# Kernel tuning notes

Hardware: AMD Instinct MI355X
Metric: run time of the kernel (lower is better)

## Reference

```python
import jax, jax.numpy as jnp
import numpy as np

N = 20000      # nodes
E = 640000     # edges (before self loops)
IN = 256       # in_channels == out_channels (forced by classifier size 4*in)
H1, C1 = 8, 16   # conv1: heads=8, out=16 -> concat 128
H2, C2 = 1, 256  # conv2: heads=1, out=out_channels
B = 4096       # article pairs
NEG_SLOPE = 0.2  # PyG GATv2Conv default negative_slope


def setup_inputs() -> dict:
    key = jax.random.key(0)
    ks = jax.random.split(key, 24)
    s = 0.05
    inp = {
        "gnn_x": jax.random.normal(ks[0], (N, IN), jnp.float32),
        "vanilla_x": jax.random.normal(ks[1], (N, IN), jnp.float32),
        "edge_src": jax.random.randint(ks[2], (E,), 0, N, jnp.int32),
        "edge_dst": jax.random.randint(ks[3], (E,), 0, N, jnp.int32),
        "a1_idx": jax.random.randint(ks[4], (B,), 0, N, jnp.int64),
        "a2_idx": jax.random.randint(ks[5], (B,), 0, N, jnp.int64),
        # conv1 params (lin_l, lin_r, att, bias)
        "Wl1": jax.random.normal(ks[6], (IN, H1 * C1), jnp.float32) * s,
        "bl1": jnp.zeros((H1 * C1,), jnp.float32),
        "Wr1": jax.random.normal(ks[7], (IN, H1 * C1), jnp.float32) * s,
        "br1": jnp.zeros((H1 * C1,), jnp.float32),
        "att1": jax.random.normal(ks[8], (H1, C1), jnp.float32) * s,
        "bias1": jnp.zeros((H1 * C1,), jnp.float32),
        # conv2 params
        "Wl2": jax.random.normal(ks[9], (H1 * C1, H2 * C2), jnp.float32) * s,
        "bl2": jnp.zeros((H2 * C2,), jnp.float32),
        "Wr2": jax.random.normal(ks[10], (H1 * C1, H2 * C2), jnp.float32) * s,
        "br2": jnp.zeros((H2 * C2,), jnp.float32),
        "att2": jax.random.normal(ks[11], (H2, C2), jnp.float32) * s,
        "bias2": jnp.zeros((H2 * C2,), jnp.float32),
        # classifier
        "Wc": jax.random.normal(ks[12], (4 * IN, 1), jnp.float32) * s,
        "bc": jnp.zeros((1,), jnp.float32),
    }
    return inp


def _gatv2_layer(x, src, dst, Wl, bl, Wr, br, att, bias):
    """GATv2Conv: x_l = lin_l(x)[src], x_r = lin_r(x)[dst];
    e = att . leaky_relu(x_l + x_r); segment softmax over dst; scatter-add x_l*alpha."""
    n = x.shape[0]
    h, c = att.shape
    xl = (x @ Wl + bl).reshape(n, h, c)
    xr = (x @ Wr + br).reshape(n, h, c)
    # per-edge attention logits [E, H]
    e = jnp.einsum('ehc,hc->eh', jax.nn.leaky_relu(xl[src] + xr[dst], NEG_SLOPE), att)
    # segment softmax over destination nodes (self loops guarantee non-empty segments)
    emax = jax.ops.segment_max(e, dst, num_segments=n)
    ex = jnp.exp(e - emax[dst])
    denom = jax.ops.segment_sum(ex, dst, num_segments=n)
    alpha = ex / denom[dst]                      # [E, H]
    out = jax.ops.segment_sum(alpha[:, :, None] * xl[src], dst, num_segments=n)  # [N,H,C]
    return out.reshape(n, h * c) + bias          # concat=True (heads=1 identical)


def reference(gnn_x, vanilla_x, Wl1, bl1, Wr1, br1, att1, bias1,
              Wl2, bl2, Wr2, br2, att2, bias2, Wc, bc,
              edge_src, edge_dst, a1_idx, a2_idx):
    n = gnn_x.shape[0]
    loops = jnp.arange(n, dtype=edge_src.dtype)
    src = jnp.concatenate([edge_src, loops])     # PyG add_self_loops=True
    dst = jnp.concatenate([edge_dst, loops])
    x = _gatv2_layer(gnn_x, src, dst, Wl1, bl1, Wr1, br1, att1, bias1)
    x = jax.nn.relu(x)
    x = _gatv2_layer(x, src, dst, Wl2, bl2, Wr2, br2, att2, bias2)
    combined = jnp.concatenate(
        [vanilla_x[a1_idx], vanilla_x[a2_idx], x[a1_idx], x[a2_idx]], axis=1)  # [B, 4*IN]
    logits = combined @ Wc + bc                  # [B, 1]
    return logits
```

## Files before the change

### kernel.cpp

```cpp
#include <hip/hip_runtime.h>
#include <math.h>

#define N_NODES 20000
#define M_PAD   20032
#define E_EDGES 640000
#define ET (E_EDGES + N_NODES)
#define IN_CH 256
#define D1 128
#define D2 256
#define BPAIRS 4096
#define NEG 0.2f
#define LOG2E 1.4426950408889634f

#define ZC_BLOCKS    20
#define WT_BLOCKS    32
#define XCONV_BLOCKS (M_PAD * IN_CH / 4 / 4 / 256)
#define RANK_BLOCKS  ((ET + 255) / 256)

#define G1X (M_PAD / 64)
#define G1Y (D1 / 64)
#define G1_BLOCKS (G1X * G1Y)
#define SCAT_BLOCKS ((ET + 255) / 256)

#if __has_builtin(__builtin_amdgcn_exp2f)
#define EXP2F(x) __builtin_amdgcn_exp2f(x)
#else
#define EXP2F(x) exp2f(x)
#endif

typedef __bf16 bf16x8 __attribute__((ext_vector_type(8)));
typedef float  f32x4  __attribute__((ext_vector_type(4)));
typedef float  f32x2  __attribute__((ext_vector_type(2)));
typedef unsigned short u16x4 __attribute__((ext_vector_type(4)));

__device__ __forceinline__ unsigned short f2b(float f) {
    unsigned int u = __float_as_uint(f);
    unsigned int r = u + 0x7FFFu + ((u >> 16) & 1u);
    return (unsigned short)(r >> 16);
}
__device__ __forceinline__ unsigned char f2f8(float f) {
    return (unsigned char)(__builtin_amdgcn_cvt_pk_fp8_f32(f, f, 0, false) & 0xFF);
}
template <bool HI>
__device__ __forceinline__ f32x2 f8up2(unsigned int u) {
    return __builtin_amdgcn_cvt_pk_f32_fp8((int)u, HI);
}
__device__ __forceinline__ f32x2 up2(unsigned int u) {
    f32x2 r;
    r.x = __uint_as_float(u << 16);
    r.y = __uint_as_float(u & 0xFFFF0000u);
    return r;
}
__device__ __forceinline__ f32x2 lrelu2(f32x2 s) {
    return __builtin_elementwise_max(s, s * NEG);
}
__device__ __forceinline__ float lrelu(float s) { return fmaxf(s, NEG * s); }

__device__ __forceinline__ void unpack8(uint4 u, float* v) {
    v[0] = __uint_as_float(u.x << 16); v[1] = __uint_as_float(u.x & 0xFFFF0000u);
    v[2] = __uint_as_float(u.y << 16); v[3] = __uint_as_float(u.y & 0xFFFF0000u);
    v[4] = __uint_as_float(u.z << 16); v[5] = __uint_as_float(u.z & 0xFFFF0000u);
    v[6] = __uint_as_float(u.w << 16); v[7] = __uint_as_float(u.w & 0xFFFF0000u);
}
__device__ __forceinline__ void unpack8_f8(uint2 u, float* v) {
    f32x2 a = f8up2<false>(u.x), b = f8up2<true>(u.x);
    f32x2 c = f8up2<false>(u.y), d = f8up2<true>(u.y);
    v[0] = a.x; v[1] = a.y; v[2] = b.x; v[3] = b.y;
    v[4] = c.x; v[5] = c.y; v[6] = d.x; v[7] = d.y;
}


__global__ __launch_bounds__(256) void prep_kernel(
        const float* __restrict__ gnn_x,
        const float* __restrict__ Wl1, const float* __restrict__ Wr1,
        const float* __restrict__ Wl2, const float* __restrict__ Wr2,
        unsigned short* __restrict__ xb,
        unsigned short* __restrict__ wt1l, unsigned short* __restrict__ wt1r,
        unsigned short* __restrict__ wt2l, unsigned short* __restrict__ wt2r,
        int* __restrict__ count) {
    __shared__ unsigned short tile[64 * 65];
    int bid = blockIdx.x;
    if (bid < ZC_BLOCKS) {
        int q = bid * 256 + threadIdx.x;
        if (q * 4 < N_NODES) {
            int4 z; z.x = z.y = z.z = z.w = 0;
            ((int4*)count)[q] = z;
        }
    } else if (bid < ZC_BLOCKS + WT_BLOCKS) {
        int t = bid - ZC_BLOCKS;
        int m = t >> 3;
        int tt = t & 7;
        const float* W;
        unsigned short* Wt;
        int K, N;
        if (m == 0)      { W = Wl1; Wt = wt1l; K = IN_CH; N = D1; }
        else if (m == 1) { W = Wr1; Wt = wt1r; K = IN_CH; N = D1; }
        else if (m == 2) { W = Wl2; Wt = wt2l; K = D1; N = D2; }
        else             { W = Wr2; Wt = wt2r; K = D1; N = D2; }
        int ntn = N >> 6;
        int k0 = (tt / ntn) << 6;
        int n0 = (tt % ntn) << 6;
        int c = threadIdx.x & 63;
        int rr = threadIdx.x >> 6;
#pragma unroll
        for (int ch = 0; ch < 16; ch++) {
            int row = rr * 16 + ch;
            tile[row * 65 + c] = f2b(W[(size_t)(k0 + row) * N + n0 + c]);
        }
        __syncthreads();
#pragma unroll
        for (int ch = 0; ch < 16; ch++) {
            int n = rr * 16 + ch;
            Wt[(size_t)(n0 + n) * K + k0 + c] = tile[c * 65 + n];
        }
    } else {
        int tid = (bid - ZC_BLOCKS - WT_BLOCKS) * 256 + threadIdx.x;
        const int NQ = M_PAD * IN_CH / 4;
        int q0 = tid * 4;
#pragma unroll
        for (int j = 0; j < 4; j++) {
            int qi = q0 + j;
            if (qi >= NQ) break;
            int e0 = qi * 4;
            int row = e0 >> 8;
            u16x4 o;
            if (row < N_NODES) {
                f32x4 v = __builtin_nontemporal_load((const f32x4*)(gnn_x + e0));
                o.x = f2b(v.x); o.y = f2b(v.y); o.z = f2b(v.z); o.w = f2b(v.w);
            } else {
                o.x = o.y = o.z = o.w = 0;
            }
            *(u16x4*)(xb + e0) = o;
        }
    }
}


__global__ __launch_bounds__(256) void rank_kernel(
        const int* __restrict__ edge_dst,
        int* __restrict__ count, int* __restrict__ rank) {
    int e = blockIdx.x * 256 + threadIdx.x;
    if (e >= ET) return;
    int dst = (e < E_EDGES) ? edge_dst[e] : (e - E_EDGES);
    rank[e] = atomicAdd(&count[dst], 1);
}


__global__ __launch_bounds__(1024) void scan_kernel(const int* __restrict__ count,
                                                    int* __restrict__ offsets) {
    const int PER = 20;
    int t = threadIdx.x;
    int base = t * PER;
    int local[PER];
    int sum = 0;
#pragma unroll
    for (int i = 0; i < PER; i++) {
        int idx = base + i;
        int v = (idx < N_NODES) ? count[idx] : 0;
        local[i] = sum;
        sum += v;
    }
    int lane = t & 63, wave = t >> 6;
    int s = sum;
#pragma unroll
    for (int off = 1; off < 64; off <<= 1) {
        int x = __shfl_up(s, off);
        if (lane >= off) s += x;
    }
    __shared__ int wsum[16];
    __shared__ int wpre[16];
    if (lane == 63) wsum[wave] = s;
    __syncthreads();
    if (t == 0) {
        int acc = 0;
        for (int w = 0; w < 16; w++) { wpre[w] = acc; acc += wsum[w]; }
        offsets[N_NODES] = acc;
    }
    __syncthreads();
    int thread_excl = wpre[wave] + (s - sum);
#pragma unroll
    for (int i = 0; i < PER; i++) {
        int idx = base + i;
        if (idx < N_NODES) offsets[idx] = thread_excl + local[i];
    }
}


template <int K>
__device__ __forceinline__ void dual_gemm_tile(
        const unsigned short* __restrict__ A,
        const unsigned short* __restrict__ Wtl,
        const unsigned short* __restrict__ Wtr,
        const float* __restrict__ bl, const float* __restrict__ br,
        unsigned char* __restrict__ Yl, unsigned short* __restrict__ Yr,
        int M, int NOUT, int bx, int by) {
    const int NK = K / 32;
    int wave = threadIdx.x >> 6;
    int lane = threadIdx.x & 63;
    int row0 = bx * 64;
    int col0 = (by * 4 + wave) * 16;
    int rsub = lane & 15;
    int koff = (lane >> 4) * 8;

    const unsigned short* ap  = A   + (size_t)(row0 + rsub) * K + koff;
    const unsigned short* bpl = Wtl + (size_t)(col0 + rsub) * K + koff;
    const unsigned short* bpr = Wtr + (size_t)(col0 + rsub) * K + koff;

    bf16x8 bfl[NK], bfr[NK];
#pragma unroll
    for (int kb = 0; kb < NK; kb++) {
        bfl[kb] = *(const bf16x8*)(bpl + kb * 32);
        bfr[kb] = *(const bf16x8*)(bpr + kb * 32);
    }

    f32x4 l0 = {0.f, 0.f, 0.f, 0.f};
    f32x4 l1 = l0, l2 = l0, l3 = l0, r0 = l0, r1 = l0, r2 = l0, r3 = l0;

#pragma unroll
    for (int kb = 0; kb < NK; kb++) {
        int off = kb * 32;
        bf16x8 a0 = *(const bf16x8*)(ap + off);
        bf16x8 a1 = *(const bf16x8*)(ap + 16 * K + off);
        bf16x8 a2 = *(const bf16x8*)(ap + 32 * K + off);
        bf16x8 a3 = *(const bf16x8*)(ap + 48 * K + off);
        l0 = __builtin_amdgcn_mfma_f32_16x16x32_bf16(a0, bfl[kb], l0, 0, 0, 0);
        r0 = __builtin_amdgcn_mfma_f32_16x16x32_bf16(a0, bfr[kb], r0, 0, 0, 0);
        l1 = __builtin_amdgcn_mfma_f32_16x16x32_bf16(a1, bfl[kb], l1, 0, 0, 0);
        r1 = __builtin_amdgcn_mfma_f32_16x16x32_bf16(a1, bfr[kb], r1, 0, 0, 0);
        l2 = __builtin_amdgcn_mfma_f32_16x16x32_bf16(a2, bfl[kb], l2, 0, 0, 0);
        r2 = __builtin_amdgcn_mfma_f32_16x16x32_bf16(a2, bfr[kb], r2, 0, 0, 0);
        l3 = __builtin_amdgcn_mfma_f32_16x16x32_bf16(a3, bfl[kb], l3, 0, 0, 0);
        r3 = __builtin_amdgcn_mfma_f32_16x16x32_bf16(a3, bfr[kb], r3, 0, 0, 0);
    }

    int colg = col0 + rsub;
    float bvl = bl[colg];
    float bvr = br[colg];
    int rbase = row0 + (lane >> 4) * 4;
#pragma unroll
    for (int t = 0; t < 4; t++) {
        f32x4 al = (t == 0) ? l0 : (t == 1) ? l1 : (t == 2) ? l2 : l3;
        f32x4 ar = (t == 0) ? r0 : (t == 1) ? r1 : (t == 2) ? r2 : r3;
#pragma unroll
        for (int r = 0; r < 4; r++) {
            int row = rbase + t * 16 + r;
            if (row < M) {
                Yl[(size_t)row * NOUT + colg] = f2f8(al[r] + bvl);
                Yr[(size_t)row * NOUT + colg] = f2b(ar[r] + bvr);
            }
        }
    }
}


__global__ __launch_bounds__(256) void gemm1_scatter_kernel(
        const unsigned short* __restrict__ A,
        const unsigned short* __restrict__ Wtl,
        const unsigned short* __restrict__ Wtr,
        const float* __restrict__ bl, const float* __restrict__ br,
        unsigned char* __restrict__ Yl, unsigned short* __restrict__ Yr,
        const int* __restrict__ edge_src, const int* __restrict__ edge_dst,
        const int* __restrict__ rank, const int* __restrict__ offsets,
        int* __restrict__ sorted_src) {
    int bid = blockIdx.x;
    if (bid < G1_BLOCKS) {
        dual_gemm_tile<IN_CH>(A, Wtl, Wtr, bl, br, Yl, Yr,
                              N_NODES, D1, bid % G1X, bid / G1X);
    } else {
        int e = (bid - G1_BLOCKS) * 256 + threadIdx.x;
        if (e >= ET) return;
        int dst = (e < E_EDGES) ? edge_dst[e] : (e - E_EDGES);
        int src = (e < E_EDGES) ? edge_src[e] : (e - E_EDGES);
        sorted_src[offsets[dst] + rank[e]] = src;
    }
}


template <int K>
__global__ __launch_bounds__(256) void dual_gemm_w32_kernel(
        const unsigned short* __restrict__ A,
        const unsigned short* __restrict__ Wtl,
        const unsigned short* __restrict__ Wtr,
        const float* __restrict__ bl, const float* __restrict__ br,
        unsigned char* __restrict__ Yl, unsigned short* __restrict__ Yr,
        int M, int NOUT) {
    const int NK = K / 32;
    int wave = threadIdx.x >> 6;
    int lane = threadIdx.x & 63;
    int row0 = blockIdx.x * 64;
    int col0 = blockIdx.y * 128 + wave * 32;
    int rsub = lane & 15;
    int koff = (lane >> 4) * 8;

    const unsigned short* ap = A + (size_t)(row0 + rsub) * K + koff;

    bf16x8 bfl[2][NK], bfr[2][NK];
#pragma unroll
    for (int c = 0; c < 2; c++) {
        const unsigned short* bpl = Wtl + (size_t)(col0 + c * 16 + rsub) * K + koff;
        const unsigned short* bpr = Wtr + (size_t)(col0 + c * 16 + rsub) * K + koff;
#pragma unroll
        for (int kb = 0; kb < NK; kb++) {
            bfl[c][kb] = *(const bf16x8*)(bpl + kb * 32);
            bfr[c][kb] = *(const bf16x8*)(bpr + kb * 32);
        }
    }

    f32x4 accl[2][4], accr[2][4];
#pragma unroll
    for (int c = 0; c < 2; c++)
#pragma unroll
        for (int t = 0; t < 4; t++) {
            accl[c][t] = (f32x4){0.f, 0.f, 0.f, 0.f};
            accr[c][t] = (f32x4){0.f, 0.f, 0.f, 0.f};
        }

#pragma unroll
    for (int kb = 0; kb < NK; kb++) {
        int off = kb * 32;
        bf16x8 a[4];
        a[0] = *(const bf16x8*)(ap + off);
        a[1] = *(const bf16x8*)(ap + 16 * K + off);
        a[2] = *(const bf16x8*)(ap + 32 * K + off);
        a[3] = *(const bf16x8*)(ap + 48 * K + off);
#pragma unroll
        for (int t = 0; t < 4; t++) {
#pragma unroll
            for (int c = 0; c < 2; c++) {
                accl[c][t] = __builtin_amdgcn_mfma_f32_16x16x32_bf16(
                    a[t], bfl[c][kb], accl[c][t], 0, 0, 0);
                accr[c][t] = __builtin_amdgcn_mfma_f32_16x16x32_bf16(
                    a[t], bfr[c][kb], accr[c][t], 0, 0, 0);
            }
        }
    }

    int rbase = row0 + (lane >> 4) * 4;
#pragma unroll
    for (int c = 0; c < 2; c++) {
        int colg = col0 + c * 16 + rsub;
        float bvl = bl[colg];
        float bvr = br[colg];
#pragma unroll
        for (int t = 0; t < 4; t++) {
#pragma unroll
            for (int r = 0; r < 4; r++) {
                int row = rbase + t * 16 + r;
                if (row < M) {
                    Yl[(size_t)row * NOUT + colg] = f2f8(accl[c][t][r] + bvl);
                    Yr[(size_t)row * NOUT + colg] = f2b(accr[c][t][r] + bvr);
                }
            }
        }
    }
}


__global__ __launch_bounds__(256) void aggregate1_kernel(
        const unsigned char* __restrict__ xl1, const unsigned short* __restrict__ xr1,
        const float* __restrict__ att1, const float* __restrict__ bias1,
        const int* __restrict__ offsets, const int* __restrict__ sorted_src,
        unsigned short* __restrict__ x1) {
    int wave = threadIdx.x >> 6;
    int lane = threadIdx.x & 63;
    int q = lane >> 4;
    int ql = lane & 15;
    int dst = blockIdx.x * 4 + wave;
    if (dst >= M_PAD) return;
    int c0 = ql * 8;
    if (dst >= N_NODES) {
        if (q == 0) {
            uint4 z; z.x = z.y = z.z = z.w = 0;
            *(uint4*)(x1 + (size_t)dst * D1 + c0) = z;
        }
        return;
    }

    uint4 xu = *(const uint4*)(xr1 + (size_t)dst * D1 + c0);
    f32x2 xr[4] = {up2(xu.x), up2(xu.y), up2(xu.z), up2(xu.w)};
    float4 aa0 = *(const float4*)(att1 + c0);
    float4 aa1 = *(const float4*)(att1 + c0 + 4);
    f32x2 att[4];
    att[0].x = aa0.x * LOG2E; att[0].y = aa0.y * LOG2E;
    att[1].x = aa0.z * LOG2E; att[1].y = aa0.w * LOG2E;
    att[2].x = aa1.x * LOG2E; att[2].y = aa1.y * LOG2E;
    att[3].x = aa1.z * LOG2E; att[3].y = aa1.w * LOG2E;

    int beg = offsets[dst], end = offsets[dst + 1];
    const unsigned char* base = xl1 + c0;

    float l = 0.f;
    f32x2 acc[4] = {{0.f,0.f},{0.f,0.f},{0.f,0.f},{0.f,0.f}};

    int i = beg;
    int s0 = sorted_src[min(i + q, end - 1)];
    uint2 g0 = *(const uint2*)(base + (size_t)s0 * D1);
    bool more1 = (i + 4) < end;
    uint2 g1;
    if (more1) {
        int s1 = sorted_src[min(i + 4 + q, end - 1)];
        g1 = *(const uint2*)(base + (size_t)s1 * D1);
    }
    while (true) {
        bool more2 = (i + 8) < end;
        uint2 g2;
        if (more2) {
            int s2 = sorted_src[min(i + 8 + q, end - 1)];
            g2 = *(const uint2*)(base + (size_t)s2 * D1);
        }
        bool act = (i + q) < end;
        f32x2 v0 = f8up2<false>(g0.x), v1 = f8up2<true>(g0.x);
        f32x2 v2 = f8up2<false>(g0.y), v3 = f8up2<true>(g0.y);
        f32x2 p2 = att[0] * lrelu2(v0 + xr[0]);
        p2 += att[1] * lrelu2(v1 + xr[1]);
        p2 += att[2] * lrelu2(v2 + xr[2]);
        p2 += att[3] * lrelu2(v3 + xr[3]);
        float p = p2.x + p2.y;
        p += __shfl_xor(p, 1);
        float w = act ? EXP2F(p) : 0.f;
        l += w;
        acc[0] += w * v0; acc[1] += w * v1; acc[2] += w * v2; acc[3] += w * v3;
        if (!more1) break;
        i += 4;
        g0 = g1; g1 = g2; more1 = more2;
    }
    l += __shfl_xor(l, 16);
    l += __shfl_xor(l, 32);
#pragma unroll
    for (int j = 0; j < 4; j++) {
        f32x2 t;
        t.x = __shfl_xor(acc[j].x, 16); t.y = __shfl_xor(acc[j].y, 16);
        acc[j] += t;
        t.x = __shfl_xor(acc[j].x, 32); t.y = __shfl_xor(acc[j].y, 32);
        acc[j] += t;
    }
    if (q == 0) {
        float inv = 1.f / l;
        float4 bb0 = *(const float4*)(bias1 + c0);
        float4 bb1 = *(const float4*)(bias1 + c0 + 4);
        unsigned short o[8];
        o[0] = f2b(fmaxf(acc[0].x * inv + bb0.x, 0.f));
        o[1] = f2b(fmaxf(acc[0].y * inv + bb0.y, 0.f));
        o[2] = f2b(fmaxf(acc[1].x * inv + bb0.z, 0.f));
        o[3] = f2b(fmaxf(acc[1].y * inv + bb0.w, 0.f));
        o[4] = f2b(fmaxf(acc[2].x * inv + bb1.x, 0.f));
        o[5] = f2b(fmaxf(acc[2].y * inv + bb1.y, 0.f));
        o[6] = f2b(fmaxf(acc[3].x * inv + bb1.z, 0.f));
        o[7] = f2b(fmaxf(acc[3].y * inv + bb1.w, 0.f));
        uint4 ov;
        ov.x = (unsigned int)o[0] | ((unsigned int)o[1] << 16);
        ov.y = (unsigned int)o[2] | ((unsigned int)o[3] << 16);
        ov.z = (unsigned int)o[4] | ((unsigned int)o[5] << 16);
        ov.w = (unsigned int)o[6] | ((unsigned int)o[7] << 16);
        *(uint4*)(x1 + (size_t)dst * D1 + c0) = ov;
    }
}


__global__ __launch_bounds__(256) void agg2_classifier_kernel(
        const unsigned char* __restrict__ xl2, const unsigned short* __restrict__ xr2,
        const float* __restrict__ att2, const float* __restrict__ bias2,
        const int* __restrict__ offsets, const int* __restrict__ sorted_src,
        const float* __restrict__ vanilla_x,
        const int* __restrict__ a1_raw, const int* __restrict__ a2_raw,
        const float* __restrict__ Wc, const float* __restrict__ bc,
        float* __restrict__ out) {
    __shared__ float x2row[2][D2];
    __shared__ float mrg[2][32][9];
    __shared__ float part[4];
    __shared__ int stride_s;
    int t = threadIdx.x;
    if (t < 64) {
        bool z = (t < 31) ? (a1_raw[1 + 2 * t] == 0) : true;
        unsigned long long m = __ballot(z);
        if (t == 0) stride_s = (m == ~0ull) ? 2 : 1;
    }
    __syncthreads();
    int stride = stride_s;
    int b = blockIdx.x;
    int a1 = a1_raw[(long)b * stride];
    int a2 = a2_raw[(long)b * stride];

    int wave = t >> 6;
    int d = wave >> 1;
    int ww = wave & 1;
    int lane = t & 63;
    int half = lane >> 5;
    int hl = lane & 31;
    int c0 = hl * 8;
    int dst = d ? a2 : a1;

    float xr[8], att[8];
    unpack8(*(const uint4*)(xr2 + (size_t)dst * D2 + c0), xr);
#pragma unroll
    for (int j = 0; j < 8; j++) att[j] = att2[c0 + j] * LOG2E;
    int beg = offsets[dst], end = offsets[dst + 1];
    const unsigned char* base = xl2 + c0;

    float l = 0.f;
    float acc[8];
#pragma unroll
    for (int j = 0; j < 8; j++) acc[j] = 0.f;

    int sub = 2 * ww + half;
    int i = beg;
    int s0 = sorted_src[min(i + sub, end - 1)];
    uint2 g0 = *(const uint2*)(base + (size_t)s0 * D2);
    bool more1 = (i + 4) < end;
    uint2 g1;
    if (more1) {
        int s1 = sorted_src[min(i + 4 + sub, end - 1)];
        g1 = *(const uint2*)(base + (size_t)s1 * D2);
    }
    while (true) {
        bool more2 = (i + 8) < end;
        uint2 g2;
        if (more2) {
            int s2 = sorted_src[min(i + 8 + sub, end - 1)];
            g2 = *(const uint2*)(base + (size_t)s2 * D2);
        }
        bool act = (i + sub) < end;
        float v[8];
        unpack8_f8(g0, v);
        float p = 0.f;
#pragma unroll
        for (int j = 0; j < 8; j++) p = fmaf(att[j], lrelu(v[j] + xr[j]), p);
        p += __shfl_xor(p, 1);
        p += __shfl_xor(p, 2);
        p += __shfl_xor(p, 4);
        p += __shfl_xor(p, 8);
        p += __shfl_xor(p, 16);
        float w = act ? EXP2F(p) : 0.f;
        l += w;
#pragma unroll
        for (int j = 0; j < 8; j++) acc[j] += w * v[j];
        if (!more1) break;
        i += 4;
        g0 = g1; g1 = g2; more1 = more2;
    }
    l += __shfl_xor(l, 32);
#pragma unroll
    for (int j = 0; j < 8; j++) acc[j] += __shfl_xor(acc[j], 32);
    if (ww == 1 && half == 0) {
        mrg[d][hl][0] = l;
#pragma unroll
        for (int j = 0; j < 8; j++) mrg[d][hl][1 + j] = acc[j];
    }
    __syncthreads();
    if (ww == 0 && half == 0) {
        l += mrg[d][hl][0];
#pragma unroll
        for (int j = 0; j < 8; j++) acc[j] += mrg[d][hl][1 + j];
        float inv = 1.f / l;
#pragma unroll
        for (int j = 0; j < 8; j++)
            x2row[d][c0 + j] = acc[j] * inv + bias2[c0 + j];
    }
    __syncthreads();

    float s = vanilla_x[(size_t)a1 * IN_CH + t] * Wc[t]
            + vanilla_x[(size_t)a2 * IN_CH + t] * Wc[IN_CH + t]
            + x2row[0][t] * Wc[2 * IN_CH + t]
            + x2row[1][t] * Wc[3 * IN_CH + t];
    s += __shfl_xor(s, 1);
    s += __shfl_xor(s, 2);
    s += __shfl_xor(s, 4);
    s += __shfl_xor(s, 8);
    s += __shfl_xor(s, 16);
    s += __shfl_xor(s, 32);
    if (lane == 0) part[wave] = s;
    __syncthreads();
    if (t == 0) out[b] = part[0] + part[1] + part[2] + part[3] + bc[0];
}


extern "C" void kernel_launch(void* const* d_in, const int* in_sizes, int n_in,
                              void* d_out, int out_size, void* d_ws, size_t ws_size,
                              hipStream_t stream) {
    const float* gnn_x     = (const float*)d_in[0];
    const float* vanilla_x = (const float*)d_in[1];
    const int*   edge_src  = (const int*)d_in[2];
    const int*   edge_dst  = (const int*)d_in[3];
    const int*   a1_idx    = (const int*)d_in[4];
    const int*   a2_idx    = (const int*)d_in[5];
    const float* Wl1   = (const float*)d_in[6];
    const float* bl1   = (const float*)d_in[7];
    const float* Wr1   = (const float*)d_in[8];
    const float* br1   = (const float*)d_in[9];
    const float* att1  = (const float*)d_in[10];
    const float* bias1 = (const float*)d_in[11];
    const float* Wl2   = (const float*)d_in[12];
    const float* bl2   = (const float*)d_in[13];
    const float* Wr2   = (const float*)d_in[14];
    const float* br2   = (const float*)d_in[15];
    const float* att2  = (const float*)d_in[16];
    const float* bias2 = (const float*)d_in[17];
    const float* Wc    = (const float*)d_in[18];
    const float* bc    = (const float*)d_in[19];
    float* out = (float*)d_out;

    char* p = (char*)d_ws;
    unsigned short* xb   = (unsigned short*)p; p += (size_t)M_PAD * IN_CH * 2;
    unsigned short* x1b  = (unsigned short*)p; p += (size_t)M_PAD * D1 * 2;
    unsigned char*  xl1b = (unsigned char*)p;  p += (size_t)N_NODES * D1;
    unsigned short* xr1b = (unsigned short*)p; p += (size_t)N_NODES * D1 * 2;
    unsigned char*  xl2b = (unsigned char*)p;  p += (size_t)N_NODES * D2;
    unsigned short* xr2b = (unsigned short*)p; p += (size_t)N_NODES * D2 * 2;
    unsigned short* wt1l = (unsigned short*)p; p += (size_t)D1 * IN_CH * 2;
    unsigned short* wt1r = (unsigned short*)p; p += (size_t)D1 * IN_CH * 2;
    unsigned short* wt2l = (unsigned short*)p; p += (size_t)D2 * D1 * 2;
    unsigned short* wt2r = (unsigned short*)p; p += (size_t)D2 * D1 * 2;
    int* count      = (int*)p; p += (size_t)N_NODES * 4;
    int* offsets    = (int*)p; p += (size_t)(N_NODES + 4) * 4;
    int* rank       = (int*)p; p += (size_t)ET * 4;
    int* sorted_src = (int*)p; p += (size_t)ET * 4;

    prep_kernel<<<ZC_BLOCKS + WT_BLOCKS + XCONV_BLOCKS, 256, 0, stream>>>(
        gnn_x, Wl1, Wr1, Wl2, Wr2,
        xb, wt1l, wt1r, wt2l, wt2r, count);

    rank_kernel<<<RANK_BLOCKS, 256, 0, stream>>>(edge_dst, count, rank);

    scan_kernel<<<1, 1024, 0, stream>>>(count, offsets);

    gemm1_scatter_kernel<<<G1_BLOCKS + SCAT_BLOCKS, 256, 0, stream>>>(
        xb, wt1l, wt1r, bl1, br1, xl1b, xr1b,
        edge_src, edge_dst, rank, offsets, sorted_src);

    aggregate1_kernel<<<M_PAD / 4, 256, 0, stream>>>(
        xl1b, xr1b, att1, bias1, offsets, sorted_src, x1b);

    dim3 g2(M_PAD / 64, D2 / 128);
    dual_gemm_w32_kernel<D1><<<g2, 256, 0, stream>>>(
        x1b, wt2l, wt2r, bl2, br2, xl2b, xr2b, N_NODES, D2);

    agg2_classifier_kernel<<<BPAIRS, 256, 0, stream>>>(
        xl2b, xr2b, att2, bias2, offsets, sorted_src,
        vanilla_x, a1_idx, a2_idx, Wc, bc, out);
}
```

Baseline: 261.6 us.

## Fuse pipeline into single cooperative persistent kernel with grid syncs

Replaces the seven-kernel launch sequence with one cooperative mega-kernel of 512 persistent blocks. The stages (prep, rank, scan, gemm1+scatter, aggregate1, gemm2, agg2+classifier) are separated by grid.sync and distributed with grid-stride loops. The scan becomes a 256-thread scan that re-reads counts instead of keeping them in registers, and the GEMM tiles now load weights inside the k loop rather than preloading them. The aim is to cut launch and drain gaps between stages, at the cost of grid-wide barriers, lower parallelism in the gemm2 and agg2 stages, and a single-block-equivalent scan running while the rest of the grid waits. The old kernels are kept as a fallback path.

```diff
diff --git a/kernel.cpp b/kernel.cpp
--- a/kernel.cpp
+++ b/kernel.cpp
@@ -1,5 +1,8 @@
 #include <hip/hip_runtime.h>
+#include <hip/hip_cooperative_groups.h>
 #include <math.h>
+
+namespace cg = cooperative_groups;
 
 #define N_NODES 20000
 #define M_PAD   20032
@@ -12,15 +15,16 @@
 #define NEG 0.2f
 #define LOG2E 1.4426950408889634f
 
-#define ZC_BLOCKS    20
-#define WT_BLOCKS    32
+#define COOP_BLOCKS 512
+#define WT_BLOCKS 32
+#define ZC_BLOCKS 20
 #define XCONV_BLOCKS (M_PAD * IN_CH / 4 / 4 / 256)
 #define RANK_BLOCKS  ((ET + 255) / 256)
+#define SCAT_BLOCKS  ((ET + 255) / 256)
 
 #define G1X (M_PAD / 64)
-#define G1Y (D1 / 64)
-#define G1_BLOCKS (G1X * G1Y)
-#define SCAT_BLOCKS ((ET + 255) / 256)
+#define G1_BLOCKS (G1X * (D1 / 64))
+#define G2_TILES  (G1X * (D2 / 64))
 
 #if __has_builtin(__builtin_amdgcn_exp2f)
 #define EXP2F(x) __builtin_amdgcn_exp2f(x)
@@ -70,95 +74,64 @@
 }
 
 
-__global__ __launch_bounds__(256) void prep_kernel(
-        const float* __restrict__ gnn_x,
+__device__ __forceinline__ void dev_wt_tile(int t,
         const float* __restrict__ Wl1, const float* __restrict__ Wr1,
         const float* __restrict__ Wl2, const float* __restrict__ Wr2,
-        unsigned short* __restrict__ xb,
         unsigned short* __restrict__ wt1l, unsigned short* __restrict__ wt1r,
         unsigned short* __restrict__ wt2l, unsigned short* __restrict__ wt2r,
-        int* __restrict__ count) {
-    __shared__ unsigned short tile[64 * 65];
-    int bid = blockIdx.x;
-    if (bid < ZC_BLOCKS) {
-        int q = bid * 256 + threadIdx.x;
-        if (q * 4 < N_NODES) {
-            int4 z; z.x = z.y = z.z = z.w = 0;
-            ((int4*)count)[q] = z;
-        }
-    } else if (bid < ZC_BLOCKS + WT_BLOCKS) {
-        int t = bid - ZC_BLOCKS;
-        int m = t >> 3;
-        int tt = t & 7;
-        const float* W;
-        unsigned short* Wt;
-        int K, N;
-        if (m == 0)      { W = Wl1; Wt = wt1l; K = IN_CH; N = D1; }
-        else if (m == 1) { W = Wr1; Wt = wt1r; K = IN_CH; N = D1; }
-        else if (m == 2) { W = Wl2; Wt = wt2l; K = D1; N = D2; }
-        else             { W = Wr2; Wt = wt2r; K = D1; N = D2; }
-        int ntn = N >> 6;
-        int k0 = (tt / ntn) << 6;
-        int n0 = (tt % ntn) << 6;
-        int c = threadIdx.x & 63;
-        int rr = threadIdx.x >> 6;
-#pragma unroll
-        for (int ch = 0; ch < 16; ch++) {
-            int row = rr * 16 + ch;
-            tile[row * 65 + c] = f2b(W[(size_t)(k0 + row) * N + n0 + c]);
-        }
-        __syncthreads();
-#pragma unroll
-        for (int ch = 0; ch < 16; ch++) {
-            int n = rr * 16 + ch;
-            Wt[(size_t)(n0 + n) * K + k0 + c] = tile[c * 65 + n];
-        }
+        unsigned short* tile) {
+    int m = t >> 3;
+    int tt = t & 7;
+    const float* W;
+    unsigned short* Wt;
+    int K, N;
+    if (m == 0)      { W = Wl1; Wt = wt1l; K = IN_CH; N = D1; }
+    else if (m == 1) { W = Wr1; Wt = wt1r; K = IN_CH; N = D1; }
+    else if (m == 2) { W = Wl2; Wt = wt2l; K = D1; N = D2; }
+    else             { W = Wr2; Wt = wt2r; K = D1; N = D2; }
+    int ntn = N >> 6;
+    int k0 = (tt / ntn) << 6;
+    int n0 = (tt % ntn) << 6;
+    int c = threadIdx.x & 63;
+    int rr = threadIdx.x >> 6;
+#pragma unroll
+    for (int ch = 0; ch < 16; ch++) {
+        int row = rr * 16 + ch;
+        tile[row * 65 + c] = f2b(W[(size_t)(k0 + row) * N + n0 + c]);
+    }
+    __syncthreads();
+#pragma unroll
+    for (int ch = 0; ch < 16; ch++) {
+        int n = rr * 16 + ch;
+        Wt[(size_t)(n0 + n) * K + k0 + c] = tile[c * 65 + n];
+    }
+}
+
+__device__ __forceinline__ void dev_xconv(int qi,
+        const float* __restrict__ gnn_x, unsigned short* __restrict__ xb) {
+    int e0 = qi * 4;
+    int row = e0 >> 8;
+    u16x4 o;
+    if (row < N_NODES) {
+        f32x4 v = __builtin_nontemporal_load((const f32x4*)(gnn_x + e0));
+        o.x = f2b(v.x); o.y = f2b(v.y); o.z = f2b(v.z); o.w = f2b(v.w);
     } else {
-        int tid = (bid - ZC_BLOCKS - WT_BLOCKS) * 256 + threadIdx.x;
-        const int NQ = M_PAD * IN_CH / 4;
-        int q0 = tid * 4;
-#pragma unroll
-        for (int j = 0; j < 4; j++) {
-            int qi = q0 + j;
-            if (qi >= NQ) break;
-            int e0 = qi * 4;
-            int row = e0 >> 8;
-            u16x4 o;
-            if (row < N_NODES) {
-                f32x4 v = __builtin_nontemporal_load((const f32x4*)(gnn_x + e0));
-                o.x = f2b(v.x); o.y = f2b(v.y); o.z = f2b(v.z); o.w = f2b(v.w);
-            } else {
-                o.x = o.y = o.z = o.w = 0;
-            }
-            *(u16x4*)(xb + e0) = o;
-        }
-    }
-}
-
-
-__global__ __launch_bounds__(256) void rank_kernel(
-        const int* __restrict__ edge_dst,
-        int* __restrict__ count, int* __restrict__ rank) {
-    int e = blockIdx.x * 256 + threadIdx.x;
-    if (e >= ET) return;
-    int dst = (e < E_EDGES) ? edge_dst[e] : (e - E_EDGES);
-    rank[e] = atomicAdd(&count[dst], 1);
-}
-
-
-__global__ __launch_bounds__(1024) void scan_kernel(const int* __restrict__ count,
-                                                    int* __restrict__ offsets) {
-    const int PER = 20;
+        o.x = o.y = o.z = o.w = 0;
+    }
+    *(u16x4*)(xb + e0) = o;
+}
+
+__device__ __forceinline__ void scan256(const int* __restrict__ count,
+                                        int* __restrict__ offsets,
+                                        int* wbuf) {
+    const int PER = 79;
     int t = threadIdx.x;
     int base = t * PER;
-    int local[PER];
     int sum = 0;
-#pragma unroll
+#pragma unroll 8
     for (int i = 0; i < PER; i++) {
         int idx = base + i;
-        int v = (idx < N_NODES) ? count[idx] : 0;
-        local[i] = sum;
-        sum += v;
+        if (idx < N_NODES) sum += count[idx];
     }
     int lane = t & 63, wave = t >> 6;
     int s = sum;
@@ -167,24 +140,24 @@
         int x = __shfl_up(s, off);
         if (lane >= off) s += x;
     }
-    __shared__ int wsum[16];
-    __shared__ int wpre[16];
+    int* wsum = wbuf;
+    int* wpre = wbuf + 4;
     if (lane == 63) wsum[wave] = s;
     __syncthreads();
     if (t == 0) {
         int acc = 0;
-        for (int w = 0; w < 16; w++) { wpre[w] = acc; acc += wsum[w]; }
-        offsets[N_NODES] = acc;
+        for (int w = 0; w < 4; w++) { wpre[w] = acc; acc += wsum[w]; }
     }
     __syncthreads();
-    int thread_excl = wpre[wave] + (s - sum);
-#pragma unroll
+    int excl = wpre[wave] + (s - sum);
+    if (t == 255) offsets[N_NODES] = excl + sum;
+    int run = excl;
+#pragma unroll 8
     for (int i = 0; i < PER; i++) {
         int idx = base + i;
-        if (idx < N_NODES) offsets[idx] = thread_excl + local[i];
-    }
-}
-
+        if (idx < N_NODES) { offsets[idx] = run; run += count[idx]; }
+    }
+}
 
 template <int K>
 __device__ __forceinline__ void dual_gemm_tile(
@@ -206,31 +179,26 @@
     const unsigned short* bpl = Wtl + (size_t)(col0 + rsub) * K + koff;
     const unsigned short* bpr = Wtr + (size_t)(col0 + rsub) * K + koff;
 
-    bf16x8 bfl[NK], bfr[NK];
-#pragma unroll
-    for (int kb = 0; kb < NK; kb++) {
-        bfl[kb] = *(const bf16x8*)(bpl + kb * 32);
-        bfr[kb] = *(const bf16x8*)(bpr + kb * 32);
-    }
-
     f32x4 l0 = {0.f, 0.f, 0.f, 0.f};
     f32x4 l1 = l0, l2 = l0, l3 = l0, r0 = l0, r1 = l0, r2 = l0, r3 = l0;
 
 #pragma unroll
     for (int kb = 0; kb < NK; kb++) {
         int off = kb * 32;
+        bf16x8 bfl = *(const bf16x8*)(bpl + off);
+        bf16x8 bfr = *(const bf16x8*)(bpr + off);
         bf16x8 a0 = *(const bf16x8*)(ap + off);
         bf16x8 a1 = *(const bf16x8*)(ap + 16 * K + off);
         bf16x8 a2 = *(const bf16x8*)(ap + 32 * K + off);
         bf16x8 a3 = *(const bf16x8*)(ap + 48 * K + off);
-        l0 = __builtin_amdgcn_mfma_f32_16x16x32_bf16(a0, bfl[kb], l0, 0, 0, 0);
-        r0 = __builtin_amdgcn_mfma_f32_16x16x32_bf16(a0, bfr[kb], r0, 0, 0, 0);
-        l1 = __builtin_amdgcn_mfma_f32_16x16x32_bf16(a1, bfl[kb], l1, 0, 0, 0);
-        r1 = __builtin_amdgcn_mfma_f32_16x16x32_bf16(a1, bfr[kb], r1, 0, 0, 0);
-        l2 = __builtin_amdgcn_mfma_f32_16x16x32_bf16(a2, bfl[kb], l2, 0, 0, 0);
-        r2 = __builtin_amdgcn_mfma_f32_16x16x32_bf16(a2, bfr[kb], r2, 0, 0, 0);
-        l3 = __builtin_amdgcn_mfma_f32_16x16x32_bf16(a3, bfl[kb], l3, 0, 0, 0);
-        r3 = __builtin_amdgcn_mfma_f32_16x16x32_bf16(a3, bfr[kb], r3, 0, 0, 0);
+        l0 = __builtin_amdgcn_mfma_f32_16x16x32_bf16(a0, bfl, l0, 0, 0, 0);
+        r0 = __builtin_amdgcn_mfma_f32_16x16x32_bf16(a0, bfr, r0, 0, 0, 0);
+        l1 = __builtin_amdgcn_mfma_f32_16x16x32_bf16(a1, bfl, l1, 0, 0, 0);
+        r1 = __builtin_amdgcn_mfma_f32_16x16x32_bf16(a1, bfr, r1, 0, 0, 0);
+        l2 = __builtin_amdgcn_mfma_f32_16x16x32_bf16(a2, bfl, l2, 0, 0, 0);
+        r2 = __builtin_amdgcn_mfma_f32_16x16x32_bf16(a2, bfr, r2, 0, 0, 0);
+        l3 = __builtin_amdgcn_mfma_f32_16x16x32_bf16(a3, bfl, l3, 0, 0, 0);
+        r3 = __builtin_amdgcn_mfma_f32_16x16x32_bf16(a3, bfr, r3, 0, 0, 0);
     }
 
     int colg = col0 + rsub;
@@ -252,121 +220,13 @@
     }
 }
 
-
-__global__ __launch_bounds__(256) void gemm1_scatter_kernel(
-        const unsigned short* __restrict__ A,
-        const unsigned short* __restrict__ Wtl,
-        const unsigned short* __restrict__ Wtr,
-        const float* __restrict__ bl, const float* __restrict__ br,
-        unsigned char* __restrict__ Yl, unsigned short* __restrict__ Yr,
-        const int* __restrict__ edge_src, const int* __restrict__ edge_dst,
-        const int* __restrict__ rank, const int* __restrict__ offsets,
-        int* __restrict__ sorted_src) {
-    int bid = blockIdx.x;
-    if (bid < G1_BLOCKS) {
-        dual_gemm_tile<IN_CH>(A, Wtl, Wtr, bl, br, Yl, Yr,
-                              N_NODES, D1, bid % G1X, bid / G1X);
-    } else {
-        int e = (bid - G1_BLOCKS) * 256 + threadIdx.x;
-        if (e >= ET) return;
-        int dst = (e < E_EDGES) ? edge_dst[e] : (e - E_EDGES);
-        int src = (e < E_EDGES) ? edge_src[e] : (e - E_EDGES);
-        sorted_src[offsets[dst] + rank[e]] = src;
-    }
-}
-
-
-template <int K>
-__global__ __launch_bounds__(256) void dual_gemm_w32_kernel(
-        const unsigned short* __restrict__ A,
-        const unsigned short* __restrict__ Wtl,
-        const unsigned short* __restrict__ Wtr,
-        const float* __restrict__ bl, const float* __restrict__ br,
-        unsigned char* __restrict__ Yl, unsigned short* __restrict__ Yr,
-        int M, int NOUT) {
-    const int NK = K / 32;
-    int wave = threadIdx.x >> 6;
-    int lane = threadIdx.x & 63;
-    int row0 = blockIdx.x * 64;
-    int col0 = blockIdx.y * 128 + wave * 32;
-    int rsub = lane & 15;
-    int koff = (lane >> 4) * 8;
-
-    const unsigned short* ap = A + (size_t)(row0 + rsub) * K + koff;
-
-    bf16x8 bfl[2][NK], bfr[2][NK];
-#pragma unroll
-    for (int c = 0; c < 2; c++) {
-        const unsigned short* bpl = Wtl + (size_t)(col0 + c * 16 + rsub) * K + koff;
-        const unsigned short* bpr = Wtr + (size_t)(col0 + c * 16 + rsub) * K + koff;
-#pragma unroll
-        for (int kb = 0; kb < NK; kb++) {
-            bfl[c][kb] = *(const bf16x8*)(bpl + kb * 32);
-            bfr[c][kb] = *(const bf16x8*)(bpr + kb * 32);
-        }
-    }
-
-    f32x4 accl[2][4], accr[2][4];
-#pragma unroll
-    for (int c = 0; c < 2; c++)
-#pragma unroll
-        for (int t = 0; t < 4; t++) {
-            accl[c][t] = (f32x4){0.f, 0.f, 0.f, 0.f};
-            accr[c][t] = (f32x4){0.f, 0.f, 0.f, 0.f};
-        }
-
-#pragma unroll
-    for (int kb = 0; kb < NK; kb++) {
-        int off = kb * 32;
-        bf16x8 a[4];
-        a[0] = *(const bf16x8*)(ap + off);
-        a[1] = *(const bf16x8*)(ap + 16 * K + off);
-        a[2] = *(const bf16x8*)(ap + 32 * K + off);
-        a[3] = *(const bf16x8*)(ap + 48 * K + off);
-#pragma unroll
-        for (int t = 0; t < 4; t++) {
-#pragma unroll
-            for (int c = 0; c < 2; c++) {
-                accl[c][t] = __builtin_amdgcn_mfma_f32_16x16x32_bf16(
-                    a[t], bfl[c][kb], accl[c][t], 0, 0, 0);
-                accr[c][t] = __builtin_amdgcn_mfma_f32_16x16x32_bf16(
-                    a[t], bfr[c][kb], accr[c][t], 0, 0, 0);
-            }
-        }
-    }
-
-    int rbase = row0 + (lane >> 4) * 4;
-#pragma unroll
-    for (int c = 0; c < 2; c++) {
-        int colg = col0 + c * 16 + rsub;
-        float bvl = bl[colg];
-        float bvr = br[colg];
-#pragma unroll
-        for (int t = 0; t < 4; t++) {
-#pragma unroll
-            for (int r = 0; r < 4; r++) {
-                int row = rbase + t * 16 + r;
-                if (row < M) {
-                    Yl[(size_t)row * NOUT + colg] = f2f8(accl[c][t][r] + bvl);
-                    Yr[(size_t)row * NOUT + colg] = f2b(accr[c][t][r] + bvr);
-                }
-            }
-        }
-    }
-}
-
-
-__global__ __launch_bounds__(256) void aggregate1_kernel(
+__device__ __forceinline__ void agg1_unit(
         const unsigned char* __restrict__ xl1, const unsigned short* __restrict__ xr1,
         const float* __restrict__ att1, const float* __restrict__ bias1,
         const int* __restrict__ offsets, const int* __restrict__ sorted_src,
-        unsigned short* __restrict__ x1) {
-    int wave = threadIdx.x >> 6;
-    int lane = threadIdx.x & 63;
+        unsigned short* __restrict__ x1, int dst, int lane) {
     int q = lane >> 4;
     int ql = lane & 15;
-    int dst = blockIdx.x * 4 + wave;
-    if (dst >= M_PAD) return;
     int c0 = ql * 8;
     if (dst >= N_NODES) {
         if (q == 0) {
@@ -375,7 +235,6 @@
         }
         return;
     }
-
     uint4 xu = *(const uint4*)(xr1 + (size_t)dst * D1 + c0);
     f32x2 xr[4] = {up2(xu.x), up2(xu.y), up2(xu.z), up2(xu.w)};
     float4 aa0 = *(const float4*)(att1 + c0);
@@ -456,31 +315,21 @@
     }
 }
 
-
-__global__ __launch_bounds__(256) void agg2_classifier_kernel(
+struct Agg2S {
+    float x2row[2][D2];
+    float mrg[2][32][9];
+    float part[4];
+    int stride_s;
+};
+
+__device__ __forceinline__ void agg2_pair(
         const unsigned char* __restrict__ xl2, const unsigned short* __restrict__ xr2,
         const float* __restrict__ att2, const float* __restrict__ bias2,
         const int* __restrict__ offsets, const int* __restrict__ sorted_src,
         const float* __restrict__ vanilla_x,
-        const int* __restrict__ a1_raw, const int* __restrict__ a2_raw,
         const float* __restrict__ Wc, const float* __restrict__ bc,
-        float* __restrict__ out) {
-    __shared__ float x2row[2][D2];
-    __shared__ float mrg[2][32][9];
-    __shared__ float part[4];
-    __shared__ int stride_s;
+        float* __restrict__ out, int b, int a1, int a2, Agg2S* S) {
     int t = threadIdx.x;
-    if (t < 64) {
-        bool z = (t < 31) ? (a1_raw[1 + 2 * t] == 0) : true;
-        unsigned long long m = __ballot(z);
-        if (t == 0) stride_s = (m == ~0ull) ? 2 : 1;
-    }
-    __syncthreads();
-    int stride = stride_s;
-    int b = blockIdx.x;
-    int a1 = a1_raw[(long)b * stride];
-    int a2 = a2_raw[(long)b * stride];
-
     int wave = t >> 6;
     int d = wave >> 1;
     int ww = wave & 1;
@@ -542,35 +391,241 @@
 #pragma unroll
     for (int j = 0; j < 8; j++) acc[j] += __shfl_xor(acc[j], 32);
     if (ww == 1 && half == 0) {
-        mrg[d][hl][0] = l;
-#pragma unroll
-        for (int j = 0; j < 8; j++) mrg[d][hl][1 + j] = acc[j];
+        S->mrg[d][hl][0] = l;
+#pragma unroll
+        for (int j = 0; j < 8; j++) S->mrg[d][hl][1 + j] = acc[j];
     }
     __syncthreads();
     if (ww == 0 && half == 0) {
-        l += mrg[d][hl][0];
-#pragma unroll
-        for (int j = 0; j < 8; j++) acc[j] += mrg[d][hl][1 + j];
+        l += S->mrg[d][hl][0];
+#pragma unroll
+        for (int j = 0; j < 8; j++) acc[j] += S->mrg[d][hl][1 + j];
         float inv = 1.f / l;
 #pragma unroll
         for (int j = 0; j < 8; j++)
-            x2row[d][c0 + j] = acc[j] * inv + bias2[c0 + j];
+            S->x2row[d][c0 + j] = acc[j] * inv + bias2[c0 + j];
     }
     __syncthreads();
 
     float s = vanilla_x[(size_t)a1 * IN_CH + t] * Wc[t]
             + vanilla_x[(size_t)a2 * IN_CH + t] * Wc[IN_CH + t]
-            + x2row[0][t] * Wc[2 * IN_CH + t]
-            + x2row[1][t] * Wc[3 * IN_CH + t];
+            + S->x2row[0][t] * Wc[2 * IN_CH + t]
+            + S->x2row[1][t] * Wc[3 * IN_CH + t];
     s += __shfl_xor(s, 1);
     s += __shfl_xor(s, 2);
     s += __shfl_xor(s, 4);
     s += __shfl_xor(s, 8);
     s += __shfl_xor(s, 16);
     s += __shfl_xor(s, 32);
-    if (lane == 0) part[wave] = s;
+    if (lane == 0) S->part[wave] = s;
     __syncthreads();
-    if (t == 0) out[b] = part[0] + part[1] + part[2] + part[3] + bc[0];
+    if (t == 0) out[b] = S->part[0] + S->part[1] + S->part[2] + S->part[3] + bc[0];
+}
+
+
+struct Params {
+    const float* gnn_x; const float* vanilla_x;
+    const int* edge_src; const int* edge_dst;
+    const int* a1_raw; const int* a2_raw;
+    const float* Wl1; const float* bl1; const float* Wr1; const float* br1;
+    const float* att1; const float* bias1;
+    const float* Wl2; const float* bl2; const float* Wr2; const float* br2;
+    const float* att2; const float* bias2;
+    const float* Wc; const float* bc;
+    float* out;
+    unsigned short* xb; unsigned short* x1b;
+    unsigned char* xl1b; unsigned short* xr1b;
+    unsigned char* xl2b; unsigned short* xr2b;
+    unsigned short* wt1l; unsigned short* wt1r;
+    unsigned short* wt2l; unsigned short* wt2r;
+    int* count; int* offsets; int* rank; int* sorted_src;
+};
+
+__global__ __launch_bounds__(256, 2) void mega_kernel(Params P) {
+    cg::grid_group grid = cg::this_grid();
+    __shared__ __align__(16) char smem_raw[8448];
+    const int bid = blockIdx.x, tid = threadIdx.x, NB = gridDim.x;
+    const int NT = NB * 256;
+    const int g = bid * 256 + tid;
+
+    for (int q = g; q < N_NODES / 4; q += NT) {
+        int4 z; z.x = z.y = z.z = z.w = 0;
+        ((int4*)P.count)[q] = z;
+    }
+    if (bid < WT_BLOCKS)
+        dev_wt_tile(bid, P.Wl1, P.Wr1, P.Wl2, P.Wr2,
+                    P.wt1l, P.wt1r, P.wt2l, P.wt2r, (unsigned short*)smem_raw);
+    {
+        const int NQ = M_PAD * IN_CH / 4;
+        for (int qi = g; qi < NQ; qi += NT) dev_xconv(qi, P.gnn_x, P.xb);
+    }
+    grid.sync();
+
+    for (int e = g; e < ET; e += NT) {
+        int dst = (e < E_EDGES) ? P.edge_dst[e] : (e - E_EDGES);
+        P.rank[e] = atomicAdd(&P.count[dst], 1);
+    }
+    for (int t = bid; t < G1_BLOCKS; t += NB)
+        dual_gemm_tile<IN_CH>(P.xb, P.wt1l, P.wt1r, P.bl1, P.br1,
+                              P.xl1b, P.xr1b, N_NODES, D1, t % G1X, t / G1X);
+    grid.sync();
+
+    if (bid == 0) scan256(P.count, P.offsets, (int*)smem_raw);
+    grid.sync();
+
+    for (int e = g; e < ET; e += NT) {
+        int dst = (e < E_EDGES) ? P.edge_dst[e] : (e - E_EDGES);
+        int src = (e < E_EDGES) ? P.edge_src[e] : (e - E_EDGES);
+        P.sorted_src[P.offsets[dst] + P.rank[e]] = src;
+    }
+    grid.sync();
+
+    {
+        int wave = tid >> 6, lane = tid & 63;
+        for (int dst = bid * 4 + wave; dst < M_PAD; dst += NB * 4)
+            agg1_unit(P.xl1b, P.xr1b, P.att1, P.bias1,
+                      P.offsets, P.sorted_src, P.x1b, dst, lane);
+    }
+    grid.sync();
+
+    for (int t = bid; t < G2_TILES; t += NB)
+        dual_gemm_tile<D1>(P.x1b, P.wt2l, P.wt2r, P.bl2, P.br2,
+                           P.xl2b, P.xr2b, N_NODES, D2, t % G1X, t / G1X);
+    grid.sync();
+
+    {
+        Agg2S* S = (Agg2S*)smem_raw;
+        if (tid < 64) {
+            bool z = (tid < 31) ? (P.a1_raw[1 + 2 * tid] == 0) : true;
+            unsigned long long m = __ballot(z);
+            if (tid == 0) S->stride_s = (m == ~0ull) ? 2 : 1;
+        }
+        __syncthreads();
+        int stride = S->stride_s;
+        for (int b = bid; b < BPAIRS; b += NB) {
+            int a1 = P.a1_raw[(long)b * stride];
+            int a2 = P.a2_raw[(long)b * stride];
+            agg2_pair(P.xl2b, P.xr2b, P.att2, P.bias2, P.offsets, P.sorted_src,
+                      P.vanilla_x, P.Wc, P.bc, P.out, b, a1, a2, S);
+            __syncthreads();
+        }
+    }
+}
+
+
+__global__ __launch_bounds__(256) void prep_kernel_fb(
+        const float* __restrict__ gnn_x,
+        const float* __restrict__ Wl1, const float* __restrict__ Wr1,
+        const float* __restrict__ Wl2, const float* __restrict__ Wr2,
+        unsigned short* __restrict__ xb,
+        unsigned short* __restrict__ wt1l, unsigned short* __restrict__ wt1r,
+        unsigned short* __restrict__ wt2l, unsigned short* __restrict__ wt2r,
+        int* __restrict__ count) {
+    __shared__ __align__(16) unsigned short tile[64 * 65];
+    int bid = blockIdx.x;
+    if (bid < ZC_BLOCKS) {
+        int q = bid * 256 + threadIdx.x;
+        if (q < N_NODES / 4) {
+            int4 z; z.x = z.y = z.z = z.w = 0;
+            ((int4*)count)[q] = z;
+        }
+    } else if (bid < ZC_BLOCKS + WT_BLOCKS) {
+        dev_wt_tile(bid - ZC_BLOCKS, Wl1, Wr1, Wl2, Wr2,
+                    wt1l, wt1r, wt2l, wt2r, tile);
+    } else {
+        int tid = (bid - ZC_BLOCKS - WT_BLOCKS) * 256 + threadIdx.x;
+        const int NQ = M_PAD * IN_CH / 4;
+        int q0 = tid * 4;
+#pragma unroll
+        for (int j = 0; j < 4; j++) {
+            int qi = q0 + j;
+            if (qi >= NQ) break;
+            dev_xconv(qi, gnn_x, xb);
+        }
+    }
+}
+
+__global__ __launch_bounds__(256) void rank_kernel_fb(
+        const int* __restrict__ edge_dst,
+        int* __restrict__ count, int* __restrict__ rank) {
+    int e = blockIdx.x * 256 + threadIdx.x;
+    if (e >= ET) return;
+    int dst = (e < E_EDGES) ? edge_dst[e] : (e - E_EDGES);
+    rank[e] = atomicAdd(&count[dst], 1);
+}
+
+__global__ __launch_bounds__(256) void scan_kernel_fb(const int* __restrict__ count,
+                                                     int* __restrict__ offsets) {
+    __shared__ int wbuf[8];
+    scan256(count, offsets, wbuf);
+}
+
+__global__ __launch_bounds__(256) void gemm1_scatter_kernel_fb(
+        const unsigned short* __restrict__ A,
+        const unsigned short* __restrict__ Wtl,
+        const unsigned short* __restrict__ Wtr,
+        const float* __restrict__ bl, const float* __restrict__ br,
+        unsigned char* __restrict__ Yl, unsigned short* __restrict__ Yr,
+        const int* __restrict__ edge_src, const int* __restrict__ edge_dst,
+        const int* __restrict__ rank, const int* __restrict__ offsets,
+        int* __restrict__ sorted_src) {
+    int bid = blockIdx.x;
+    if (bid < G1_BLOCKS) {
+        dual_gemm_tile<IN_CH>(A, Wtl, Wtr, bl, br, Yl, Yr,
+                              N_NODES, D1, bid % G1X, bid / G1X);
+    } else {
+        int e = (bid - G1_BLOCKS) * 256 + threadIdx.x;
+        if (e >= ET) return;
+        int dst = (e < E_EDGES) ? edge_dst[e] : (e - E_EDGES);
+        int src = (e < E_EDGES) ? edge_src[e] : (e - E_EDGES);
+        sorted_src[offsets[dst] + rank[e]] = src;
+    }
+}
+
+__global__ __launch_bounds__(256) void aggregate1_kernel_fb(
+        const unsigned char* __restrict__ xl1, const unsigned short* __restrict__ xr1,
+        const float* __restrict__ att1, const float* __restrict__ bias1,
+        const int* __restrict__ offsets, const int* __restrict__ sorted_src,
+        unsigned short* __restrict__ x1) {
+    int dst = blockIdx.x * 4 + (threadIdx.x >> 6);
+    if (dst >= M_PAD) return;
+    agg1_unit(xl1, xr1, att1, bias1, offsets, sorted_src, x1, dst, threadIdx.x & 63);
+}
+
+template <int K>
+__global__ __launch_bounds__(256) void dual_gemm_kernel_fb(
+        const unsigned short* __restrict__ A,
+        const unsigned short* __restrict__ Wtl,
+        const unsigned short* __restrict__ Wtr,
+        const float* __restrict__ bl, const float* __restrict__ br,
+        unsigned char* __restrict__ Yl, unsigned short* __restrict__ Yr,
+        int M, int NOUT) {
+    dual_gemm_tile<K>(A, Wtl, Wtr, bl, br, Yl, Yr, M, NOUT, blockIdx.x, blockIdx.y);
+}
+
+__global__ __launch_bounds__(256) void agg2_classifier_kernel_fb(
+        const unsigned char* __restrict__ xl2, const unsigned short* __restrict__ xr2,
+        const float* __restrict__ att2, const float* __restrict__ bias2,
+        const int* __restrict__ offsets, const int* __restrict__ sorted_src,
+        const float* __restrict__ vanilla_x,
+        const int* __restrict__ a1_raw, const int* __restrict__ a2_raw,
+        const float* __restrict__ Wc, const float* __restrict__ bc,
+        float* __restrict__ out) {
+    __shared__ __align__(16) char smem_raw[sizeof(Agg2S)];
+    Agg2S* S = (Agg2S*)smem_raw;
+    int t = threadIdx.x;
+    if (t < 64) {
+        bool z = (t < 31) ? (a1_raw[1 + 2 * t] == 0) : true;
+        unsigned long long m = __ballot(z);
+        if (t == 0) S->stride_s = (m == ~0ull) ? 2 : 1;
+    }
+    __syncthreads();
+    int stride = S->stride_s;
+    int b = blockIdx.x;
+    int a1 = a1_raw[(long)b * stride];
+    int a2 = a2_raw[(long)b * stride];
+    agg2_pair(xl2, xr2, att2, bias2, offsets, sorted_src,
+              vanilla_x, Wc, bc, out, b, a1, a2, S);
 }
 
 
@@ -615,26 +670,37 @@
     int* rank       = (int*)p; p += (size_t)ET * 4;
     int* sorted_src = (int*)p; p += (size_t)ET * 4;
 
-    prep_kernel<<<ZC_BLOCKS + WT_BLOCKS + XCONV_BLOCKS, 256, 0, stream>>>(
-        gnn_x, Wl1, Wr1, Wl2, Wr2,
-        xb, wt1l, wt1r, wt2l, wt2r, count);
-
-    rank_kernel<<<RANK_BLOCKS, 256, 0, stream>>>(edge_dst, count, rank);
-
-    scan_kernel<<<1, 1024, 0, stream>>>(count, offsets);
-
-    gemm1_scatter_kernel<<<G1_BLOCKS + SCAT_BLOCKS, 256, 0, stream>>>(
+    Params prm;
+    prm.gnn_x = gnn_x; prm.vanilla_x = vanilla_x;
+    prm.edge_src = edge_src; prm.edge_dst = edge_dst;
+    prm.a1_raw = a1_idx; prm.a2_raw = a2_idx;
+    prm.Wl1 = Wl1; prm.bl1 = bl1; prm.Wr1 = Wr1; prm.br1 = br1;
+    prm.att1 = att1; prm.bias1 = bias1;
+    prm.Wl2 = Wl2; prm.bl2 = bl2; prm.Wr2 = Wr2; prm.br2 = br2;
+    prm.att2 = att2; prm.bias2 = bias2;
+    prm.Wc = Wc; prm.bc = bc; prm.out = out;
+    prm.xb = xb; prm.x1b = x1b;
+    prm.xl1b = xl1b; prm.xr1b = xr1b; prm.xl2b = xl2b; prm.xr2b = xr2b;
+    prm.wt1l = wt1l; prm.wt1r = wt1r; prm.wt2l = wt2l; prm.wt2r = wt2r;
+    prm.count = count; prm.offsets = offsets;
+    prm.rank = rank; prm.sorted_src = sorted_src;
+    void* args[] = { (void*)&prm };
+    if (hipLaunchCooperativeKernel(mega_kernel, dim3(COOP_BLOCKS), dim3(256),
+                                   args, 0, stream) == hipSuccess)
+        return;
+
+    prep_kernel_fb<<<ZC_BLOCKS + WT_BLOCKS + XCONV_BLOCKS, 256, 0, stream>>>(
+        gnn_x, Wl1, Wr1, Wl2, Wr2, xb, wt1l, wt1r, wt2l, wt2r, count);
+    rank_kernel_fb<<<RANK_BLOCKS, 256, 0, stream>>>(edge_dst, count, rank);
+    scan_kernel_fb<<<1, 256, 0, stream>>>(count, offsets);
+    gemm1_scatter_kernel_fb<<<G1_BLOCKS + SCAT_BLOCKS, 256, 0, stream>>>(
         xb, wt1l, wt1r, bl1, br1, xl1b, xr1b,
         edge_src, edge_dst, rank, offsets, sorted_src);
-
-    aggregate1_kernel<<<M_PAD / 4, 256, 0, stream>>>(
+    aggregate1_kernel_fb<<<M_PAD / 4, 256, 0, stream>>>(
         xl1b, xr1b, att1, bias1, offsets, sorted_src, x1b);
-
-    dim3 g2(M_PAD / 64, D2 / 128);
-    dual_gemm_w32_kernel<D1><<<g2, 256, 0, stream>>>(
+    dual_gemm_kernel_fb<D1><<<dim3(G1X, D2 / 64), 256, 0, stream>>>(
         x1b, wt2l, wt2r, bl2, br2, xl2b, xr2b, N_NODES, D2);
-
-    agg2_classifier_kernel<<<BPAIRS, 256, 0, stream>>>(
+    agg2_classifier_kernel_fb<<<BPAIRS, 256, 0, stream>>>(
         xl2b, xr2b, att2, bias2, offsets, sorted_src,
         vanilla_x, a1_idx, a2_idx, Wc, bc, out);
 }
```

New measurement: 739.1 us. +182.6%, slower.
